# Performance work log

Measured on AMD Instinct MI355X. Metric: run time of the kernel, lower is better.

The kernel has to match this reference:

```python
import jax, jax.numpy as jnp
import numpy as np

N_TOKENS = 65536      # flattened latent vectors (z.view(-1, D))
LATENT_DIM = 256      # embedding_dim
NUM_EMBEDDINGS = 4096 # codebook size


def setup_inputs() -> dict:
    key = jax.random.key(0)
    k1, k2 = jax.random.split(key)
    z = jax.random.normal(k1, (N_TOKENS, LATENT_DIM), dtype=jnp.float32)
    embedding = jax.random.normal(k2, (NUM_EMBEDDINGS, LATENT_DIM), dtype=jnp.float32)
    return {"z": z, "embedding": embedding}


def reference(z, embedding):
    # z: [N, D], embedding: [K, D]
    # squared L2 distances: ||z||^2 - 2 z e^T + ||e||^2  -> [N, K]
    z_flat = z.reshape(-1, embedding.shape[1])
    distances = (
        jnp.sum(z_flat * z_flat, axis=1, keepdims=True)
        - 2.0 * (z_flat @ embedding.T)
        + jnp.sum(embedding * embedding, axis=1)
    )
    indices = jnp.argmin(distances, axis=1)           # [N]
    z_quantized = embedding[indices].reshape(z.shape)  # gather + reshape
    return z_quantized, indices
```

## Files before the change

kernel.cpp:

```cpp
#include <hip/hip_runtime.h>

#define NTOK 65536
#define DIMS 256
#define NCODES 4096
#define KP 24
#define MT 128
#define NT 128
#define MARGIN 0.005f
#define FLTMAX 3.402823466e38f

typedef short short8 __attribute__((ext_vector_type(8)));
typedef unsigned short us8 __attribute__((ext_vector_type(8)));
typedef float v4f __attribute__((ext_vector_type(4)));

#define ZF_OFF ((size_t)0)
#define ZF_BYTES ((size_t)NTOK * 768 * 2)
#define EF_OFF (ZF_OFF + ZF_BYTES)
#define EF_BYTES ((size_t)NCODES * 768 * 2)
#define ZN_OFF (EF_OFF + EF_BYTES)
#define ZN_BYTES ((size_t)NTOK * 4)
#define EN_OFF (ZN_OFF + ZN_BYTES)
#define EN_BYTES ((size_t)NCODES * 4)
#define CT_OFF (EN_OFF + EN_BYTES)
#define WL_OFF (CT_OFF + 256)
#define WL_BYTES ((size_t)NTOK * 4)
#define WS_REQ (WL_OFF + WL_BYTES)

__device__ __forceinline__ unsigned short f2bf(float f) {
  unsigned u = __float_as_uint(f);
  return (unsigned short)((u + 0x7FFFu + ((u >> 16) & 1u)) >> 16);
}
__device__ __forceinline__ float bf2f(unsigned short h) {
  return __uint_as_float(((unsigned)h) << 16);
}

__device__ __forceinline__ void async16(const unsigned short* g,
                                        unsigned short* l) {
  __builtin_amdgcn_global_load_lds(
      (const __attribute__((address_space(1))) unsigned int*)g,
      (__attribute__((address_space(3))) unsigned int*)l, 16, 0, 0);
}

__global__ void row_norm_kernel(const float* __restrict__ x,
                                float* __restrict__ out, int rows) {
  int wid = (blockIdx.x * blockDim.x + threadIdx.x) >> 6;
  int lane = threadIdx.x & 63;
  if (wid >= rows) return;
  const float* r = x + (size_t)wid * DIMS;
  float s = 0.f;
#pragma unroll
  for (int i = 0; i < DIMS / 64; ++i) {
    float v = r[lane + 64 * i];
    s += v * v;
  }
#pragma unroll
  for (int off = 32; off >= 1; off >>= 1) s += __shfl_down(s, off, 64);
  if (lane == 0) out[wid] = s;
}

__global__ __launch_bounds__(256) void split_frag_kernel(
    const float* __restrict__ x, unsigned short* __restrict__ xf, int off_hi2,
    int off_lo) {
  int g = blockIdx.x * 256 + threadIdx.x;
  int rl = g & 15;
  int quad = (g >> 4) & 3;
  int k32 = (g >> 6) & 7;
  int rb = g >> 9;
  int row = rb * 16 + rl;
  int k = k32 * 32 + quad * 8;
  const float* src = x + (size_t)row * DIMS + k;
  float4 f0 = *(const float4*)src;
  float4 f1 = *(const float4*)(src + 4);
  float v[8] = {f0.x, f0.y, f0.z, f0.w, f1.x, f1.y, f1.z, f1.w};
  us8 hi, lo;
#pragma unroll
  for (int i = 0; i < 8; ++i) {
    unsigned short h = f2bf(v[i]);
    hi[i] = h;
    lo[i] = f2bf(v[i] - bf2f(h));
  }
  size_t base = (size_t)rb * KP * 64 + rl + quad * 16;
  us8* dst = (us8*)xf;
  dst[base + (size_t)k32 * 64] = hi;
  dst[base + (size_t)(k32 + off_hi2) * 64] = hi;
  dst[base + (size_t)(k32 + off_lo) * 64] = lo;
}

__global__ void zero_counter_kernel(int* c) { *c = 0; }

__global__ __launch_bounds__(256, 2) void vq_mfma_kernel(
    const unsigned short* __restrict__ zf, const unsigned short* __restrict__ ef,
    const float* __restrict__ emb, const float* __restrict__ znorm,
    const float* __restrict__ enorm, float* __restrict__ out_zq,
    float* __restrict__ out_idx, int* __restrict__ wl_count,
    int* __restrict__ wl) {
  __shared__ unsigned short Abuf[24 * 512];
  __shared__ unsigned short Bbuf[24 * 512];
  __shared__ float red_bv[2][128];
  __shared__ float red_sv[2][128];
  __shared__ int red_bi[2][128];
  __shared__ int sidx[128];
  __shared__ float sznorm[128];

  const int t = threadIdx.x;
  const int w = t >> 6, lane = t & 63;
  const int wm = w >> 1, wn = w & 1;
  const int quad = lane >> 4, l15 = lane & 15;
  const int m0 = blockIdx.x * MT;

  if (t < MT) sznorm[t] = znorm[m0 + t];

  int aoff[6], boff[6];
  int ldsoff[6];
#pragma unroll
  for (int q = 0; q < 6; ++q) {
    int c = w * 6 + q;
    int tbl = c / 3, kk = c - tbl * 3;
    aoff[q] = (((blockIdx.x * 8 + tbl) * KP + kk) * 64 + lane) * 8;
    boff[q] = ((tbl * KP + kk) * 64 + lane) * 8;
    ldsoff[q] = c * 512;
  }

  float bv[16], sv[16];
  int bi[16];
#pragma unroll
  for (int s = 0; s < 16; ++s) {
    bv[s] = FLTMAX;
    sv[s] = FLTMAX;
    bi[s] = 0;
  }

  for (int n0i = 0; n0i < 32; ++n0i) {
    const size_t ebase = (size_t)(n0i * 8) * KP * 512;
    v4f acc[4][4];
#pragma unroll
    for (int i = 0; i < 4; ++i)
#pragma unroll
      for (int j = 0; j < 4; ++j) acc[i][j] = (v4f){0.f, 0.f, 0.f, 0.f};

    for (int s = 0; s < 8; ++s) {
      const int koff = s * 1536;
      __syncthreads();
#pragma unroll
      for (int q = 0; q < 6; ++q) {
        async16(zf + (size_t)aoff[q] + koff, &Abuf[ldsoff[q]]);
        async16(ef + ebase + boff[q] + koff, &Bbuf[ldsoff[q]]);
      }
      __syncthreads();
#pragma unroll
      for (int ks = 0; ks < 3; ++ks) {
        short8 af[4], bfr[4];
#pragma unroll
        for (int i = 0; i < 4; ++i)
          af[i] = *(const short8*)&Abuf[(((wm * 4 + i) * 3 + ks) * 64 + lane) * 8];
#pragma unroll
        for (int j = 0; j < 4; ++j)
          bfr[j] = *(const short8*)&Bbuf[(((wn * 4 + j) * 3 + ks) * 64 + lane) * 8];
#pragma unroll
        for (int i = 0; i < 4; ++i)
#pragma unroll
          for (int j = 0; j < 4; ++j)
            acc[i][j] = __builtin_amdgcn_mfma_f32_16x16x32_bf16(
                af[i], bfr[j], acc[i][j], 0, 0, 0);
      }
    }

    float znl[16];
#pragma unroll
    for (int i = 0; i < 4; ++i)
#pragma unroll
      for (int r = 0; r < 4; ++r)
        znl[i * 4 + r] = sznorm[wm * 64 + i * 16 + quad * 4 + r];

    const int n0 = n0i * NT;
#pragma unroll
    for (int j = 0; j < 4; ++j) {
      int code = n0 + wn * 64 + j * 16 + l15;
      float en = enorm[code];
#pragma unroll
      for (int i = 0; i < 4; ++i) {
#pragma unroll
        for (int r = 0; r < 4; ++r) {
          int slot = i * 4 + r;
          float d = (znl[slot] - 2.0f * acc[i][j][r]) + en;
          if (d < bv[slot]) {
            sv[slot] = bv[slot];
            bv[slot] = d;
            bi[slot] = code;
          } else if (d < sv[slot]) {
            sv[slot] = d;
          }
        }
      }
    }
  }

#pragma unroll
  for (int o = 1; o < 16; o <<= 1) {
#pragma unroll
    for (int s = 0; s < 16; ++s) {
      float ob = __shfl_xor(bv[s], o, 64);
      float os = __shfl_xor(sv[s], o, 64);
      int oi = __shfl_xor(bi[s], o, 64);
      bool take = (ob < bv[s]) || (ob == bv[s] && oi < bi[s]);
      float loser = take ? bv[s] : ob;
      float mins = fminf(sv[s], os);
      if (take) {
        bv[s] = ob;
        bi[s] = oi;
      }
      sv[s] = fminf(loser, mins);
    }
  }
  if (l15 == 0) {
#pragma unroll
    for (int i = 0; i < 4; ++i)
#pragma unroll
      for (int r = 0; r < 4; ++r) {
        int tl = wm * 64 + i * 16 + quad * 4 + r;
        red_bv[wn][tl] = bv[i * 4 + r];
        red_sv[wn][tl] = sv[i * 4 + r];
        red_bi[wn][tl] = bi[i * 4 + r];
      }
  }
  __syncthreads();
  if (t < MT) {
    float b0 = red_bv[0][t], b1 = red_bv[1][t];
    int i0 = red_bi[0][t], i1 = red_bi[1][t];
    float s0 = red_sv[0][t], s1 = red_sv[1][t];
    bool take = (b1 < b0) || (b1 == b0 && i1 < i0);
    float bb = take ? b1 : b0;
    int bidx = take ? i1 : i0;
    float ss = fminf(fminf(s0, s1), take ? b0 : b1);
    out_idx[m0 + t] = (float)bidx;
    sidx[t] = bidx;
    if (ss - bb < MARGIN) {
      int slot = atomicAdd(wl_count, 1);
      if (slot < NTOK) wl[slot] = m0 + t;
    }
  }
  __syncthreads();
  {
    int row = t >> 1, half = t & 1;
    int src = sidx[row];
    const float4* sp = (const float4*)(emb + (size_t)src * DIMS + half * 128);
    float4* dp = (float4*)(out_zq + (size_t)(m0 + row) * DIMS + half * 128);
#pragma unroll
    for (int qq = 0; qq < 32; ++qq) dp[qq] = sp[qq];
  }
}

__global__ __launch_bounds__(256) void rescue_kernel(
    const float* __restrict__ z, const float* __restrict__ emb,
    const float* __restrict__ znorm, const float* __restrict__ enorm,
    const int* __restrict__ wl_count, const int* __restrict__ wl,
    float* __restrict__ out_zq, float* __restrict__ out_idx) {
  __shared__ __align__(16) float zrow[256];
  __shared__ float rv[256];
  __shared__ int ri[256];
  __shared__ int s_best;
  int n = *wl_count;
  if (n > NTOK) n = NTOK;
  for (int e = blockIdx.x; e < n; e += gridDim.x) {
    int token = wl[e];
    __syncthreads();
    zrow[threadIdx.x] = z[(size_t)token * DIMS + threadIdx.x];
    __syncthreads();
    float zn = znorm[token];
    float bvv = FLTMAX;
    int bii = 0;
    for (int c = threadIdx.x; c < NCODES; c += 256) {
      const float4* er = (const float4*)(emb + (size_t)c * DIMS);
      float dot = 0.f;
#pragma unroll 16
      for (int q = 0; q < 64; ++q) {
        float4 ev = er[q];
        float4 zv = *(const float4*)&zrow[q * 4];
        dot += ev.x * zv.x + ev.y * zv.y + ev.z * zv.z + ev.w * zv.w;
      }
      float d = (zn - 2.0f * dot) + enorm[c];
      if (d < bvv) {
        bvv = d;
        bii = c;
      }
    }
    rv[threadIdx.x] = bvv;
    ri[threadIdx.x] = bii;
    __syncthreads();
    if (threadIdx.x == 0) {
      float bb = rv[0];
      int bx = ri[0];
      for (int q = 1; q < 256; ++q) {
        float v = rv[q];
        int ix = ri[q];
        if (v < bb || (v == bb && ix < bx)) {
          bb = v;
          bx = ix;
        }
      }
      out_idx[token] = (float)bx;
      s_best = bx;
    }
    __syncthreads();
    out_zq[(size_t)token * DIMS + threadIdx.x] =
        emb[(size_t)s_best * DIMS + threadIdx.x];
  }
}

__global__ __launch_bounds__(256) void vq_argmin_legacy(
    const float* __restrict__ z, const float* __restrict__ emb,
    const float* __restrict__ znorm, const float* __restrict__ enorm,
    float* __restrict__ out_zq, float* __restrict__ out_idx) {
  __shared__ float As[32][128];
  __shared__ float Bs[32][128];
  __shared__ float red_v[128][17];
  __shared__ int red_i[128][17];
  const int t = threadIdx.x;
  const int tx = t & 15, ty = t >> 4;
  const int m0 = blockIdx.x * 128;
  int rows[8];
#pragma unroll
  for (int i = 0; i < 8; ++i)
    rows[i] = (i < 4) ? (ty * 4 + i) : (64 + ty * 4 + (i - 4));
  float zn[8];
#pragma unroll
  for (int i = 0; i < 8; ++i) zn[i] = znorm[m0 + rows[i]];
  float bestv[8];
  int besti[8];
#pragma unroll
  for (int i = 0; i < 8; ++i) {
    bestv[i] = FLTMAX;
    besti[i] = 0;
  }
  const int lrow = t >> 1;
  const int lhalf = t & 1;
  const float* zsrc_base = z + (size_t)(m0 + lrow) * DIMS + lhalf * 16;
  for (int n0 = 0; n0 < NCODES; n0 += 128) {
    float acc[8][8];
#pragma unroll
    for (int i = 0; i < 8; ++i)
#pragma unroll
      for (int j = 0; j < 8; ++j) acc[i][j] = 0.f;
    const float* esrc_base = emb + (size_t)(n0 + lrow) * DIMS + lhalf * 16;
    for (int k0 = 0; k0 < DIMS; k0 += 32) {
      __syncthreads();
      {
        const float4* s4 = (const float4*)(zsrc_base + k0);
        float4 v0 = s4[0], v1 = s4[1], v2 = s4[2], v3 = s4[3];
        int kb = lhalf * 16;
        float vv[16] = {v0.x, v0.y, v0.z, v0.w, v1.x, v1.y, v1.z, v1.w,
                        v2.x, v2.y, v2.z, v2.w, v3.x, v3.y, v3.z, v3.w};
#pragma unroll
        for (int q = 0; q < 16; ++q) As[kb + q][lrow] = vv[q];
      }
      {
        const float4* s4 = (const float4*)(esrc_base + k0);
        float4 v0 = s4[0], v1 = s4[1], v2 = s4[2], v3 = s4[3];
        int kb = lhalf * 16;
        float vv[16] = {v0.x, v0.y, v0.z, v0.w, v1.x, v1.y, v1.z, v1.w,
                        v2.x, v2.y, v2.z, v2.w, v3.x, v3.y, v3.z, v3.w};
#pragma unroll
        for (int q = 0; q < 16; ++q) Bs[kb + q][lrow] = vv[q];
      }
      __syncthreads();
#pragma unroll 8
      for (int k = 0; k < 32; ++k) {
        float4 a0 = *(const float4*)&As[k][ty * 4];
        float4 a1 = *(const float4*)&As[k][64 + ty * 4];
        float4 b0 = *(const float4*)&Bs[k][tx * 4];
        float4 b1 = *(const float4*)&Bs[k][64 + tx * 4];
        float a[8] = {a0.x, a0.y, a0.z, a0.w, a1.x, a1.y, a1.z, a1.w};
        float b[8] = {b0.x, b0.y, b0.z, b0.w, b1.x, b1.y, b1.z, b1.w};
#pragma unroll
        for (int i = 0; i < 8; ++i)
#pragma unroll
          for (int j = 0; j < 8; ++j) acc[i][j] += a[i] * b[j];
      }
    }
#pragma unroll
    for (int j = 0; j < 8; ++j) {
      int col = n0 + ((j < 4) ? (tx * 4 + j) : (64 + tx * 4 + (j - 4)));
      float en = enorm[col];
#pragma unroll
      for (int i = 0; i < 8; ++i) {
        float d = (zn[i] - 2.0f * acc[i][j]) + en;
        if (d < bestv[i]) {
          bestv[i] = d;
          besti[i] = col;
        }
      }
    }
  }
#pragma unroll
  for (int i = 0; i < 8; ++i) {
    red_v[rows[i]][tx] = bestv[i];
    red_i[rows[i]][tx] = besti[i];
  }
  __syncthreads();
  if (t < 128) {
    float bvv = red_v[t][0];
    int bii = red_i[t][0];
#pragma unroll
    for (int c = 1; c < 16; ++c) {
      float v = red_v[t][c];
      int ix = red_i[t][c];
      if (v < bvv || (v == bvv && ix < bii)) {
        bvv = v;
        bii = ix;
      }
    }
    out_idx[m0 + t] = (float)bii;
    red_i[t][16] = bii;
  }
  __syncthreads();
  {
    int grow = t >> 1, gh = t & 1;
    int src = red_i[grow][16];
    const float4* sp = (const float4*)(emb + (size_t)src * DIMS + gh * 128);
    float4* dp = (float4*)(out_zq + (size_t)(m0 + grow) * DIMS + gh * 128);
#pragma unroll
    for (int q = 0; q < 32; ++q) dp[q] = sp[q];
  }
}

extern "C" void kernel_launch(void* const* d_in, const int* in_sizes, int n_in,
                              void* d_out, int out_size, void* d_ws,
                              size_t ws_size, hipStream_t stream) {
  const float* z = (const float*)d_in[0];
  const float* emb = (const float*)d_in[1];
  float* out = (float*)d_out;
  float* out_zq = out;
  float* out_idx = out + (size_t)NTOK * DIMS;

  if (ws_size >= WS_REQ) {
    char* ws = (char*)d_ws;
    unsigned short* zf = (unsigned short*)(ws + ZF_OFF);
    unsigned short* ef = (unsigned short*)(ws + EF_OFF);
    float* znorm = (float*)(ws + ZN_OFF);
    float* enorm = (float*)(ws + EN_OFF);
    int* wl_count = (int*)(ws + CT_OFF);
    int* wl = (int*)(ws + WL_OFF);

    split_frag_kernel<<<NTOK / 8, 256, 0, stream>>>(z, zf, 8, 16);
    split_frag_kernel<<<NCODES / 8, 256, 0, stream>>>(emb, ef, 16, 8);
    row_norm_kernel<<<NCODES / 4, 256, 0, stream>>>(emb, enorm, NCODES);
    row_norm_kernel<<<NTOK / 4, 256, 0, stream>>>(z, znorm, NTOK);
    zero_counter_kernel<<<1, 1, 0, stream>>>(wl_count);
    vq_mfma_kernel<<<NTOK / MT, 256, 0, stream>>>(zf, ef, emb, znorm, enorm,
                                                  out_zq, out_idx, wl_count, wl);
    rescue_kernel<<<128, 256, 0, stream>>>(z, emb, znorm, enorm, wl_count, wl,
                                           out_zq, out_idx);
  } else {
    float* enorm = (float*)d_ws;
    float* znorm = enorm + NCODES;
    row_norm_kernel<<<NCODES / 4, 256, 0, stream>>>(emb, enorm, NCODES);
    row_norm_kernel<<<NTOK / 4, 256, 0, stream>>>(z, znorm, NTOK);
    vq_argmin_legacy<<<NTOK / 128, 256, 0, stream>>>(z, emb, znorm, enorm,
                                                     out_zq, out_idx);
  }
}
```

Before: 982.2 us.

## Restructure VQ pipeline: 3-term bf16 split, codebook-split grid, packed keys, batched rescue

```diff
diff --git a/kernel.cpp b/kernel.cpp
--- a/kernel.cpp
+++ b/kernel.cpp
@@ -1,27 +1,28 @@
 #include <hip/hip_runtime.h>
+
+typedef unsigned int u32;
+typedef unsigned long long u64;
+typedef short short8 __attribute__((ext_vector_type(8)));
+typedef unsigned short us8 __attribute__((ext_vector_type(8)));
+typedef float v4f __attribute__((ext_vector_type(4)));
 
 #define NTOK 65536
 #define DIMS 256
 #define NCODES 4096
-#define KP 24
-#define MT 128
-#define NT 128
-#define MARGIN 0.005f
+#define MARGIN 0.02f
 #define FLTMAX 3.402823466e38f
 
-typedef short short8 __attribute__((ext_vector_type(8)));
-typedef unsigned short us8 __attribute__((ext_vector_type(8)));
-typedef float v4f __attribute__((ext_vector_type(4)));
-
 #define ZF_OFF ((size_t)0)
-#define ZF_BYTES ((size_t)NTOK * 768 * 2)
+#define ZF_BYTES ((size_t)NTOK * 512 * 2)
 #define EF_OFF (ZF_OFF + ZF_BYTES)
-#define EF_BYTES ((size_t)NCODES * 768 * 2)
-#define ZN_OFF (EF_OFF + EF_BYTES)
-#define ZN_BYTES ((size_t)NTOK * 4)
-#define EN_OFF (ZN_OFF + ZN_BYTES)
+#define EF_BYTES ((size_t)NCODES * 512 * 2)
+#define EN_OFF (EF_OFF + EF_BYTES)
 #define EN_BYTES ((size_t)NCODES * 4)
-#define CT_OFF (EN_OFF + EN_BYTES)
+#define MK_OFF (EN_OFF + EN_BYTES)
+#define MK_BYTES ((size_t)4 * NTOK * 8)
+#define MSV_OFF (MK_OFF + MK_BYTES)
+#define MSV_BYTES ((size_t)4 * NTOK * 4)
+#define CT_OFF (MSV_OFF + MSV_BYTES)
 #define WL_OFF (CT_OFF + 256)
 #define WL_BYTES ((size_t)NTOK * 4)
 #define WS_REQ (WL_OFF + WL_BYTES)
@@ -33,12 +34,313 @@
 __device__ __forceinline__ float bf2f(unsigned short h) {
   return __uint_as_float(((unsigned)h) << 16);
 }
+__device__ __forceinline__ u32 umin32(u32 a, u32 b) { return a < b ? a : b; }
+__device__ __forceinline__ u32 umax32(u32 a, u32 b) { return a > b ? a : b; }
 
 __device__ __forceinline__ void async16(const unsigned short* g,
                                         unsigned short* l) {
   __builtin_amdgcn_global_load_lds(
       (const __attribute__((address_space(1))) unsigned int*)g,
       (__attribute__((address_space(3))) unsigned int*)l, 16, 0, 0);
+}
+
+__global__ __launch_bounds__(256) void split_kernel(
+    const float* __restrict__ x, unsigned short* __restrict__ xf,
+    float* __restrict__ norm_out, int* __restrict__ zero_me) {
+  const int t = threadIdx.x;
+  if (zero_me && blockIdx.x == 0 && t == 0) *zero_me = 0;
+  const int row = blockIdx.x * 64 + (t >> 2);
+  const int q = t & 3;
+  const int rb = row >> 4, rl = row & 15;
+  const float* src = x + (size_t)row * DIMS + q * 64;
+  us8* dst = (us8*)xf;
+  const size_t base = (size_t)rb * 1024 + rl;
+  float s = 0.f;
+#pragma unroll
+  for (int o = 0; o < 8; ++o) {
+    float4 f0 = ((const float4*)src)[o * 2];
+    float4 f1 = ((const float4*)src)[o * 2 + 1];
+    float v[8] = {f0.x, f0.y, f0.z, f0.w, f1.x, f1.y, f1.z, f1.w};
+    us8 hi, lo;
+#pragma unroll
+    for (int i = 0; i < 8; ++i) {
+      unsigned short h = f2bf(v[i]);
+      hi[i] = h;
+      lo[i] = f2bf(v[i] - bf2f(h));
+      s += v[i] * v[i];
+    }
+    int k32l = q * 2 + (o >> 2);
+    int qp = o & 3;
+    dst[base + (size_t)k32l * 64 + 16 * qp] = hi;
+    dst[base + (size_t)(k32l + 8) * 64 + 16 * qp] = lo;
+  }
+  if (norm_out) {
+    s += __shfl_xor(s, 1, 64);
+    s += __shfl_xor(s, 2, 64);
+    if (q == 0) norm_out[row] = s + 1024.0f;
+  }
+}
+
+__global__ __launch_bounds__(256, 3) void vq_mfma_kernel(
+    const unsigned short* __restrict__ zf, const unsigned short* __restrict__ ef,
+    const float* __restrict__ enorm, u64* __restrict__ mkey,
+    u32* __restrict__ msv) {
+  __shared__ short8 AS[1024];
+  __shared__ short8 BS[1024];
+  __shared__ u64 red_key[2][128];
+  __shared__ u32 red_sv[2][128];
+
+  const int t = threadIdx.x;
+  const int w = t >> 6, lane = t & 63;
+  const int wm = w >> 1, wn = w & 1;
+  const int quad = lane >> 4, l15 = lane & 15;
+  const int bid = blockIdx.x;
+  const int half = bid >> 9;
+  const int mb = bid & 511;
+
+  const unsigned short* baseA[4];
+  const unsigned short* baseB[4];
+#pragma unroll
+  for (int q = 0; q < 4; ++q) {
+    int ib = 2 * w + (q >> 1);
+    baseA[q] = zf + ((size_t)(mb * 8 + ib) * 16) * 512 + lane * 8;
+    baseB[q] = ef + ((size_t)(half * 64 + ib) * 16) * 512 + lane * 8;
+  }
+
+  u32 bv[16], sv[16];
+#pragma unroll
+  for (int s = 0; s < 16; ++s) {
+    bv[s] = 0xFFFFFFFFu;
+    sv[s] = 0xFFFFFFFFu;
+  }
+
+#pragma unroll 1
+  for (int n0i = 0; n0i < 8; ++n0i) {
+    float en[4];
+#pragma unroll
+    for (int j = 0; j < 4; ++j)
+      en[j] = enorm[half * 1024 + n0i * 128 + wn * 64 + j * 16 + l15];
+
+    v4f acc[4][4];
+#pragma unroll
+    for (int i = 0; i < 4; ++i)
+#pragma unroll
+      for (int j = 0; j < 4; ++j) acc[i][j] = (v4f){0.f, 0.f, 0.f, 0.f};
+
+#pragma unroll
+    for (int s = 0; s < 12; ++s) {
+      const int pkz = (s < 4) ? 2 * s : 2 * s - 8;
+      const int pke = (s < 8) ? 2 * s : 2 * s - 16;
+      __syncthreads();
+#pragma unroll
+      for (int q = 0; q < 4; ++q) {
+        async16(baseA[q] + (pkz + (q & 1)) * 512,
+                (unsigned short*)&AS[(w * 4 + q) * 64]);
+        async16(baseB[q] + (pke + (q & 1)) * 512,
+                (unsigned short*)&BS[(w * 4 + q) * 64]);
+      }
+      __syncthreads();
+#pragma unroll
+      for (int ks = 0; ks < 2; ++ks) {
+        short8 af[4], bf[4];
+#pragma unroll
+        for (int i = 0; i < 4; ++i)
+          af[i] = AS[((wm * 4 + i) * 2 + ks) * 64 + lane];
+#pragma unroll
+        for (int j = 0; j < 4; ++j)
+          bf[j] = BS[((wn * 4 + j) * 2 + ks) * 64 + lane];
+#pragma unroll
+        for (int i = 0; i < 4; ++i)
+#pragma unroll
+          for (int j = 0; j < 4; ++j)
+            acc[i][j] = __builtin_amdgcn_mfma_f32_16x16x32_bf16(
+                af[i], bf[j], acc[i][j], 0, 0, 0);
+      }
+    }
+
+#pragma unroll
+    for (int j = 0; j < 4; ++j) {
+      const u32 lid = (u32)(n0i * 4 + j);
+      const float enj = en[j];
+#pragma unroll
+      for (int i = 0; i < 4; ++i)
+#pragma unroll
+        for (int r = 0; r < 4; ++r) {
+          float d = fmaf(acc[i][j][r], -2.0f, enj);
+          u32 key = (__float_as_uint(d) & 0xFFFFFFE0u) | lid;
+          int s = i * 4 + r;
+          u32 mx = umax32(bv[s], key);
+          bv[s] = umin32(bv[s], key);
+          sv[s] = umin32(sv[s], mx);
+        }
+    }
+
+#pragma unroll
+    for (int q = 0; q < 4; ++q) baseB[q] += 8 * 16 * 512;
+  }
+
+#pragma unroll
+  for (int s = 0; s < 16; ++s) {
+    u32 val = bv[s] & 0xFFFFFFE0u;
+    u32 lid = bv[s] & 31u;
+    u32 code = half * 1024 + ((lid >> 2) << 7) + (wn << 6) + ((lid & 3) << 4) +
+               l15;
+    u64 k = ((u64)val << 12) | code;
+    u32 svv = sv[s] & 0xFFFFFFE0u;
+#pragma unroll
+    for (int o = 1; o < 16; o <<= 1) {
+      u32 klo = __shfl_xor((u32)k, o, 64);
+      u32 khi = __shfl_xor((u32)(k >> 32), o, 64);
+      u64 ok = ((u64)khi << 32) | klo;
+      u32 osv = __shfl_xor(svv, o, 64);
+      u64 mx = k > ok ? k : ok;
+      k = k < ok ? k : ok;
+      svv = umin32(umin32(svv, osv), (u32)(mx >> 12));
+    }
+    if (l15 == 0) {
+      int row = wm * 64 + (s >> 2) * 16 + quad * 4 + (s & 3);
+      red_key[wn][row] = k;
+      red_sv[wn][row] = svv;
+    }
+  }
+  __syncthreads();
+  if (t < 128) {
+    u64 k0 = red_key[0][t], k1 = red_key[1][t];
+    u64 mx = k0 > k1 ? k0 : k1;
+    u64 b = k0 < k1 ? k0 : k1;
+    u32 s = umin32(umin32(red_sv[0][t], red_sv[1][t]), (u32)(mx >> 12));
+    size_t tok = (size_t)mb * 128 + t;
+    mkey[(size_t)half * NTOK + tok] = b;
+    msv[(size_t)half * NTOK + tok] = s;
+  }
+}
+
+__global__ __launch_bounds__(256) void merge_kernel(
+    const u64* __restrict__ mkey, const u32* __restrict__ msv,
+    const float* __restrict__ emb, float* __restrict__ out_zq,
+    float* __restrict__ out_idx, int* __restrict__ wl_count,
+    int* __restrict__ wl) {
+  __shared__ int sidx[128];
+  const int t = threadIdx.x;
+  const int tok0 = blockIdx.x * 128;
+  if (t < 128) {
+    int tok = tok0 + t;
+    u64 b = mkey[tok];
+    u32 s = msv[tok];
+#pragma unroll
+    for (int h = 1; h < 4; ++h) {
+      u64 kh = mkey[(size_t)h * NTOK + tok];
+      u32 sh = msv[(size_t)h * NTOK + tok];
+      u64 mx = b > kh ? b : kh;
+      b = b < kh ? b : kh;
+      s = umin32(umin32(s, sh), (u32)(mx >> 12));
+    }
+    int code = (int)(b & 0xFFFu);
+    out_idx[tok] = (float)code;
+    sidx[t] = code;
+    float gap = __uint_as_float(s) - __uint_as_float((u32)(b >> 12));
+    if (gap < MARGIN) {
+      int sl = atomicAdd(wl_count, 1);
+      if (sl < NTOK) wl[sl] = tok;
+    }
+  }
+  __syncthreads();
+  {
+    int row = t >> 1, hf = t & 1;
+    int src = sidx[row];
+    const float4* sp = (const float4*)(emb + (size_t)src * DIMS + hf * 128);
+    float4* dp = (float4*)(out_zq + (size_t)(tok0 + row) * DIMS + hf * 128);
+#pragma unroll
+    for (int qd = 0; qd < 32; ++qd) dp[qd] = sp[qd];
+  }
+}
+
+__global__ __launch_bounds__(256) void rescue_kernel(
+    const float* __restrict__ z, const float* __restrict__ emb,
+    const float* __restrict__ enorm_b, const int* __restrict__ wl_count,
+    const int* __restrict__ wl, float* __restrict__ out_zq,
+    float* __restrict__ out_idx) {
+  __shared__ __align__(16) float zr[4][256];
+  __shared__ float rv[4][4];
+  __shared__ int ri[4][4];
+  __shared__ int sbest[4];
+  const int t = threadIdx.x;
+  const int wv = t >> 6, lane = t & 63;
+  int n = *wl_count;
+  if (n > NTOK) n = NTOK;
+  for (int base = blockIdx.x * 4; base < n; base += 256 * 4) {
+    int cnt = n - base;
+    if (cnt > 4) cnt = 4;
+    __syncthreads();
+    for (int b2 = 0; b2 < cnt; ++b2)
+      zr[b2][t] = z[(size_t)wl[base + b2] * DIMS + t];
+    __syncthreads();
+    float bvv[4] = {FLTMAX, FLTMAX, FLTMAX, FLTMAX};
+    int bii[4] = {0, 0, 0, 0};
+    for (int k = 0; k < 16; ++k) {
+      int c = k * 256 + t;
+      const float4* er = (const float4*)(emb + (size_t)c * DIMS);
+      float d0 = 0.f, d1 = 0.f, d2 = 0.f, d3 = 0.f;
+#pragma unroll 8
+      for (int qd = 0; qd < 64; ++qd) {
+        float4 ev = er[qd];
+        float4 z0 = *(const float4*)&zr[0][qd * 4];
+        float4 z1 = *(const float4*)&zr[1][qd * 4];
+        float4 z2 = *(const float4*)&zr[2][qd * 4];
+        float4 z3 = *(const float4*)&zr[3][qd * 4];
+        d0 += ev.x * z0.x + ev.y * z0.y + ev.z * z0.z + ev.w * z0.w;
+        d1 += ev.x * z1.x + ev.y * z1.y + ev.z * z1.z + ev.w * z1.w;
+        d2 += ev.x * z2.x + ev.y * z2.y + ev.z * z2.z + ev.w * z2.w;
+        d3 += ev.x * z3.x + ev.y * z3.y + ev.z * z3.z + ev.w * z3.w;
+      }
+      float en = enorm_b[c];
+      float dd[4] = {en - 2.f * d0, en - 2.f * d1, en - 2.f * d2,
+                     en - 2.f * d3};
+#pragma unroll
+      for (int b2 = 0; b2 < 4; ++b2)
+        if (dd[b2] < bvv[b2]) {
+          bvv[b2] = dd[b2];
+          bii[b2] = c;
+        }
+    }
+#pragma unroll
+    for (int b2 = 0; b2 < 4; ++b2) {
+      float v = bvv[b2];
+      int ix = bii[b2];
+      for (int off = 32; off >= 1; off >>= 1) {
+        float ov = __shfl_down(v, off, 64);
+        int oi = __shfl_down(ix, off, 64);
+        if (ov < v || (ov == v && oi < ix)) {
+          v = ov;
+          ix = oi;
+        }
+      }
+      if (lane == 0) {
+        rv[b2][wv] = v;
+        ri[b2][wv] = ix;
+      }
+    }
+    __syncthreads();
+    if (t < cnt) {
+      float v = rv[t][0];
+      int ix = ri[t][0];
+#pragma unroll
+      for (int q = 1; q < 4; ++q) {
+        float ov = rv[t][q];
+        int oi = ri[t][q];
+        if (ov < v || (ov == v && oi < ix)) {
+          v = ov;
+          ix = oi;
+        }
+      }
+      out_idx[wl[base + t]] = (float)ix;
+      sbest[t] = ix;
+    }
+    __syncthreads();
+    for (int b2 = 0; b2 < cnt; ++b2)
+      out_zq[(size_t)wl[base + b2] * DIMS + t] =
+          emb[(size_t)sbest[b2] * DIMS + t];
+  }
 }
 
 __global__ void row_norm_kernel(const float* __restrict__ x,
@@ -58,259 +360,10 @@
   if (lane == 0) out[wid] = s;
 }
 
-__global__ __launch_bounds__(256) void split_frag_kernel(
-    const float* __restrict__ x, unsigned short* __restrict__ xf, int off_hi2,
-    int off_lo) {
-  int g = blockIdx.x * 256 + threadIdx.x;
-  int rl = g & 15;
-  int quad = (g >> 4) & 3;
-  int k32 = (g >> 6) & 7;
-  int rb = g >> 9;
-  int row = rb * 16 + rl;
-  int k = k32 * 32 + quad * 8;
-  const float* src = x + (size_t)row * DIMS + k;
-  float4 f0 = *(const float4*)src;
-  float4 f1 = *(const float4*)(src + 4);
-  float v[8] = {f0.x, f0.y, f0.z, f0.w, f1.x, f1.y, f1.z, f1.w};
-  us8 hi, lo;
-#pragma unroll
-  for (int i = 0; i < 8; ++i) {
-    unsigned short h = f2bf(v[i]);
-    hi[i] = h;
-    lo[i] = f2bf(v[i] - bf2f(h));
-  }
-  size_t base = (size_t)rb * KP * 64 + rl + quad * 16;
-  us8* dst = (us8*)xf;
-  dst[base + (size_t)k32 * 64] = hi;
-  dst[base + (size_t)(k32 + off_hi2) * 64] = hi;
-  dst[base + (size_t)(k32 + off_lo) * 64] = lo;
-}
-
-__global__ void zero_counter_kernel(int* c) { *c = 0; }
-
-__global__ __launch_bounds__(256, 2) void vq_mfma_kernel(
-    const unsigned short* __restrict__ zf, const unsigned short* __restrict__ ef,
-    const float* __restrict__ emb, const float* __restrict__ znorm,
-    const float* __restrict__ enorm, float* __restrict__ out_zq,
-    float* __restrict__ out_idx, int* __restrict__ wl_count,
-    int* __restrict__ wl) {
-  __shared__ unsigned short Abuf[24 * 512];
-  __shared__ unsigned short Bbuf[24 * 512];
-  __shared__ float red_bv[2][128];
-  __shared__ float red_sv[2][128];
-  __shared__ int red_bi[2][128];
-  __shared__ int sidx[128];
-  __shared__ float sznorm[128];
-
-  const int t = threadIdx.x;
-  const int w = t >> 6, lane = t & 63;
-  const int wm = w >> 1, wn = w & 1;
-  const int quad = lane >> 4, l15 = lane & 15;
-  const int m0 = blockIdx.x * MT;
-
-  if (t < MT) sznorm[t] = znorm[m0 + t];
-
-  int aoff[6], boff[6];
-  int ldsoff[6];
-#pragma unroll
-  for (int q = 0; q < 6; ++q) {
-    int c = w * 6 + q;
-    int tbl = c / 3, kk = c - tbl * 3;
-    aoff[q] = (((blockIdx.x * 8 + tbl) * KP + kk) * 64 + lane) * 8;
-    boff[q] = ((tbl * KP + kk) * 64 + lane) * 8;
-    ldsoff[q] = c * 512;
-  }
-
-  float bv[16], sv[16];
-  int bi[16];
-#pragma unroll
-  for (int s = 0; s < 16; ++s) {
-    bv[s] = FLTMAX;
-    sv[s] = FLTMAX;
-    bi[s] = 0;
-  }
-
-  for (int n0i = 0; n0i < 32; ++n0i) {
-    const size_t ebase = (size_t)(n0i * 8) * KP * 512;
-    v4f acc[4][4];
-#pragma unroll
-    for (int i = 0; i < 4; ++i)
-#pragma unroll
-      for (int j = 0; j < 4; ++j) acc[i][j] = (v4f){0.f, 0.f, 0.f, 0.f};
-
-    for (int s = 0; s < 8; ++s) {
-      const int koff = s * 1536;
-      __syncthreads();
-#pragma unroll
-      for (int q = 0; q < 6; ++q) {
-        async16(zf + (size_t)aoff[q] + koff, &Abuf[ldsoff[q]]);
-        async16(ef + ebase + boff[q] + koff, &Bbuf[ldsoff[q]]);
-      }
-      __syncthreads();
-#pragma unroll
-      for (int ks = 0; ks < 3; ++ks) {
-        short8 af[4], bfr[4];
-#pragma unroll
-        for (int i = 0; i < 4; ++i)
-          af[i] = *(const short8*)&Abuf[(((wm * 4 + i) * 3 + ks) * 64 + lane) * 8];
-#pragma unroll
-        for (int j = 0; j < 4; ++j)
-          bfr[j] = *(const short8*)&Bbuf[(((wn * 4 + j) * 3 + ks) * 64 + lane) * 8];
-#pragma unroll
-        for (int i = 0; i < 4; ++i)
-#pragma unroll
-          for (int j = 0; j < 4; ++j)
-            acc[i][j] = __builtin_amdgcn_mfma_f32_16x16x32_bf16(
-                af[i], bfr[j], acc[i][j], 0, 0, 0);
-      }
-    }
-
-    float znl[16];
-#pragma unroll
-    for (int i = 0; i < 4; ++i)
-#pragma unroll
-      for (int r = 0; r < 4; ++r)
-        znl[i * 4 + r] = sznorm[wm * 64 + i * 16 + quad * 4 + r];
-
-    const int n0 = n0i * NT;
-#pragma unroll
-    for (int j = 0; j < 4; ++j) {
-      int code = n0 + wn * 64 + j * 16 + l15;
-      float en = enorm[code];
-#pragma unroll
-      for (int i = 0; i < 4; ++i) {
-#pragma unroll
-        for (int r = 0; r < 4; ++r) {
-          int slot = i * 4 + r;
-          float d = (znl[slot] - 2.0f * acc[i][j][r]) + en;
-          if (d < bv[slot]) {
-            sv[slot] = bv[slot];
-            bv[slot] = d;
-            bi[slot] = code;
-          } else if (d < sv[slot]) {
-            sv[slot] = d;
-          }
-        }
-      }
-    }
-  }
-
-#pragma unroll
-  for (int o = 1; o < 16; o <<= 1) {
-#pragma unroll
-    for (int s = 0; s < 16; ++s) {
-      float ob = __shfl_xor(bv[s], o, 64);
-      float os = __shfl_xor(sv[s], o, 64);
-      int oi = __shfl_xor(bi[s], o, 64);
-      bool take = (ob < bv[s]) || (ob == bv[s] && oi < bi[s]);
-      float loser = take ? bv[s] : ob;
-      float mins = fminf(sv[s], os);
-      if (take) {
-        bv[s] = ob;
-        bi[s] = oi;
-      }
-      sv[s] = fminf(loser, mins);
-    }
-  }
-  if (l15 == 0) {
-#pragma unroll
-    for (int i = 0; i < 4; ++i)
-#pragma unroll
-      for (int r = 0; r < 4; ++r) {
-        int tl = wm * 64 + i * 16 + quad * 4 + r;
-        red_bv[wn][tl] = bv[i * 4 + r];
-        red_sv[wn][tl] = sv[i * 4 + r];
-        red_bi[wn][tl] = bi[i * 4 + r];
-      }
-  }
-  __syncthreads();
-  if (t < MT) {
-    float b0 = red_bv[0][t], b1 = red_bv[1][t];
-    int i0 = red_bi[0][t], i1 = red_bi[1][t];
-    float s0 = red_sv[0][t], s1 = red_sv[1][t];
-    bool take = (b1 < b0) || (b1 == b0 && i1 < i0);
-    float bb = take ? b1 : b0;
-    int bidx = take ? i1 : i0;
-    float ss = fminf(fminf(s0, s1), take ? b0 : b1);
-    out_idx[m0 + t] = (float)bidx;
-    sidx[t] = bidx;
-    if (ss - bb < MARGIN) {
-      int slot = atomicAdd(wl_count, 1);
-      if (slot < NTOK) wl[slot] = m0 + t;
-    }
-  }
-  __syncthreads();
-  {
-    int row = t >> 1, half = t & 1;
-    int src = sidx[row];
-    const float4* sp = (const float4*)(emb + (size_t)src * DIMS + half * 128);
-    float4* dp = (float4*)(out_zq + (size_t)(m0 + row) * DIMS + half * 128);
-#pragma unroll
-    for (int qq = 0; qq < 32; ++qq) dp[qq] = sp[qq];
-  }
-}
-
-__global__ __launch_bounds__(256) void rescue_kernel(
-    const float* __restrict__ z, const float* __restrict__ emb,
-    const float* __restrict__ znorm, const float* __restrict__ enorm,
-    const int* __restrict__ wl_count, const int* __restrict__ wl,
-    float* __restrict__ out_zq, float* __restrict__ out_idx) {
-  __shared__ __align__(16) float zrow[256];
-  __shared__ float rv[256];
-  __shared__ int ri[256];
-  __shared__ int s_best;
-  int n = *wl_count;
-  if (n > NTOK) n = NTOK;
-  for (int e = blockIdx.x; e < n; e += gridDim.x) {
-    int token = wl[e];
-    __syncthreads();
-    zrow[threadIdx.x] = z[(size_t)token * DIMS + threadIdx.x];
-    __syncthreads();
-    float zn = znorm[token];
-    float bvv = FLTMAX;
-    int bii = 0;
-    for (int c = threadIdx.x; c < NCODES; c += 256) {
-      const float4* er = (const float4*)(emb + (size_t)c * DIMS);
-      float dot = 0.f;
-#pragma unroll 16
-      for (int q = 0; q < 64; ++q) {
-        float4 ev = er[q];
-        float4 zv = *(const float4*)&zrow[q * 4];
-        dot += ev.x * zv.x + ev.y * zv.y + ev.z * zv.z + ev.w * zv.w;
-      }
-      float d = (zn - 2.0f * dot) + enorm[c];
-      if (d < bvv) {
-        bvv = d;
-        bii = c;
-      }
-    }
-    rv[threadIdx.x] = bvv;
-    ri[threadIdx.x] = bii;
-    __syncthreads();
-    if (threadIdx.x == 0) {
-      float bb = rv[0];
-      int bx = ri[0];
-      for (int q = 1; q < 256; ++q) {
-        float v = rv[q];
-        int ix = ri[q];
-        if (v < bb || (v == bb && ix < bx)) {
-          bb = v;
-          bx = ix;
-        }
-      }
-      out_idx[token] = (float)bx;
-      s_best = bx;
-    }
-    __syncthreads();
-    out_zq[(size_t)token * DIMS + threadIdx.x] =
-        emb[(size_t)s_best * DIMS + threadIdx.x];
-  }
-}
-
 __global__ __launch_bounds__(256) void vq_argmin_legacy(
     const float* __restrict__ z, const float* __restrict__ emb,
-    const float* __restrict__ znorm, const float* __restrict__ enorm,
-    float* __restrict__ out_zq, float* __restrict__ out_idx) {
+    const float* __restrict__ enorm, float* __restrict__ out_zq,
+    float* __restrict__ out_idx) {
   __shared__ float As[32][128];
   __shared__ float Bs[32][128];
   __shared__ float red_v[128][17];
@@ -318,13 +371,6 @@
   const int t = threadIdx.x;
   const int tx = t & 15, ty = t >> 4;
   const int m0 = blockIdx.x * 128;
-  int rows[8];
-#pragma unroll
-  for (int i = 0; i < 8; ++i)
-    rows[i] = (i < 4) ? (ty * 4 + i) : (64 + ty * 4 + (i - 4));
-  float zn[8];
-#pragma unroll
-  for (int i = 0; i < 8; ++i) zn[i] = znorm[m0 + rows[i]];
   float bestv[8];
   int besti[8];
 #pragma unroll
@@ -383,7 +429,9 @@
       float en = enorm[col];
 #pragma unroll
       for (int i = 0; i < 8; ++i) {
-        float d = (zn[i] - 2.0f * acc[i][j]) + en;
+        int rowi = (i < 4) ? (ty * 4 + i) : (64 + ty * 4 + (i - 4));
+        (void)rowi;
+        float d = en - 2.0f * acc[i][j];
         if (d < bestv[i]) {
           bestv[i] = d;
           besti[i] = col;
@@ -393,8 +441,9 @@
   }
 #pragma unroll
   for (int i = 0; i < 8; ++i) {
-    red_v[rows[i]][tx] = bestv[i];
-    red_i[rows[i]][tx] = besti[i];
+    int rowi = (i < 4) ? (ty * 4 + i) : (64 + ty * 4 + (i - 4));
+    red_v[rowi][tx] = bestv[i];
+    red_i[rowi][tx] = besti[i];
   }
   __syncthreads();
   if (t < 128) {
@@ -436,26 +485,23 @@
     char* ws = (char*)d_ws;
     unsigned short* zf = (unsigned short*)(ws + ZF_OFF);
     unsigned short* ef = (unsigned short*)(ws + EF_OFF);
-    float* znorm = (float*)(ws + ZN_OFF);
     float* enorm = (float*)(ws + EN_OFF);
+    u64* mkey = (u64*)(ws + MK_OFF);
+    u32* msv = (u32*)(ws + MSV_OFF);
     int* wl_count = (int*)(ws + CT_OFF);
     int* wl = (int*)(ws + WL_OFF);
 
-    split_frag_kernel<<<NTOK / 8, 256, 0, stream>>>(z, zf, 8, 16);
-    split_frag_kernel<<<NCODES / 8, 256, 0, stream>>>(emb, ef, 16, 8);
-    row_norm_kernel<<<NCODES / 4, 256, 0, stream>>>(emb, enorm, NCODES);
-    row_norm_kernel<<<NTOK / 4, 256, 0, stream>>>(z, znorm, NTOK);
-    zero_counter_kernel<<<1, 1, 0, stream>>>(wl_count);
-    vq_mfma_kernel<<<NTOK / MT, 256, 0, stream>>>(zf, ef, emb, znorm, enorm,
-                                                  out_zq, out_idx, wl_count, wl);
-    rescue_kernel<<<128, 256, 0, stream>>>(z, emb, znorm, enorm, wl_count, wl,
-                                           out_zq, out_idx);
+    split_kernel<<<NTOK / 64, 256, 0, stream>>>(z, zf, nullptr, nullptr);
+    split_kernel<<<NCODES / 64, 256, 0, stream>>>(emb, ef, enorm, wl_count);
+    vq_mfma_kernel<<<2048, 256, 0, stream>>>(zf, ef, enorm, mkey, msv);
+    merge_kernel<<<NTOK / 128, 256, 0, stream>>>(mkey, msv, emb, out_zq,
+                                                 out_idx, wl_count, wl);
+    rescue_kernel<<<256, 256, 0, stream>>>(z, emb, enorm, wl_count, wl, out_zq,
+                                           out_idx);
   } else {
     float* enorm = (float*)d_ws;
-    float* znorm = enorm + NCODES;
     row_norm_kernel<<<NCODES / 4, 256, 0, stream>>>(emb, enorm, NCODES);
-    row_norm_kernel<<<NTOK / 4, 256, 0, stream>>>(z, znorm, NTOK);
-    vq_argmin_legacy<<<NTOK / 128, 256, 0, stream>>>(z, emb, znorm, enorm,
-                                                     out_zq, out_idx);
-  }
-}
+    vq_argmin_legacy<<<NTOK / 128, 256, 0, stream>>>(z, emb, enorm, out_zq,
+                                                     out_idx);
+  }
+}
```

Result: slower. 1.071 ms (+9.0%).
